# Performance work log

Measured on AMD Instinct MI355X. Metric: run time of the kernel, lower is better.

The kernel has to match this reference:

```python
import jax, jax.numpy as jnp
import numpy as np

B, H, W, D = 8, 32, 32, 384      # batch, height, width, channels (=dim)
E, HID, O = 8, 1536, 384         # num_experts, mlp hidden (dim*4), out_dim
TOP_K = 2


def setup_inputs() -> dict:
    key = jax.random.key(0)
    ks = jax.random.split(key, 5)
    x = jax.random.normal(ks[0], (B, H, W, D), dtype=jnp.float32)
    # router (noise_linear unused: eval path, train=False)
    Wg = 0.02 * jax.random.normal(ks[1], (D, E), dtype=jnp.float32)
    bg = jnp.zeros((E,), dtype=jnp.float32)
    # per-expert MLP params stacked along expert axis
    W1 = 0.02 * jax.random.normal(ks[2], (E, D, HID), dtype=jnp.float32)
    b1 = jnp.zeros((E, HID), dtype=jnp.float32)
    W2 = 0.02 * jax.random.normal(ks[3], (E, HID, O), dtype=jnp.float32)
    b2 = jnp.zeros((E, O), dtype=jnp.float32)
    return {"x": x, "Wg": Wg, "bg": bg, "W1": W1, "b1": b1, "W2": W2, "b2": b2}


def reference(x, Wg, bg, W1, b1, W2, b2):
    # --- NoisyTopkRouter (eval: train=False -> no noise branch) ---
    logits = jnp.einsum('bhwd,de->bhwe', x, Wg) + bg            # [B,H,W,E]
    _, top_idx = jax.lax.top_k(logits, TOP_K)                   # [B,H,W,K]
    # mask of selected experts; sparse logits = logits where selected, -inf else
    sel = jnp.sum(jax.nn.one_hot(top_idx, E, dtype=jnp.float32), axis=-2) > 0
    sparse_logits = jnp.where(sel, logits, -jnp.inf)
    gates = jax.nn.softmax(sparse_logits, axis=-1)              # zero on non-top-k

    # --- experts: since gate is exactly 0 off the top-k, the masked
    # gather-MLP-scatter loop equals a gate-weighted sum of all expert MLPs ---
    h = jnp.einsum('bhwd,edf->bhwef', x, W1) + b1               # [B,H,W,E,HID]
    h = jax.nn.gelu(h, approximate=False)                       # torch nn.GELU = exact
    y = jnp.einsum('bhwef,efo->bhweo', h, W2) + b2              # [B,H,W,E,O]
    out = jnp.einsum('bhweo,bhwe->bhwo', y, gates)              # [B,H,W,O]
    return out
```

## Files before the change

kernel.cpp:

```cpp
#include <hip/hip_runtime.h>
#include <cmath>

#define N_TOK 8192
#define DIM   384
#define NEXP  8
#define HID   1536
#define OUTD  384
#define CAP_MT 72
#define CAP_TOK 2304
#define CAP_TB 18

typedef __attribute__((ext_vector_type(8)))  __bf16 bf16x8;
typedef __attribute__((ext_vector_type(16))) float  f32x16;
typedef __attribute__((ext_vector_type(4)))  float  f32x4;
typedef __attribute__((ext_vector_type(8)))  unsigned short u16x8;

__device__ __forceinline__ unsigned short f2bf(float f) {
    unsigned u = __float_as_uint(f);
    u += 0x7FFF + ((u >> 16) & 1);
    return (unsigned short)(u >> 16);
}

__device__ __forceinline__ float bf2f(unsigned short s) {
    return __uint_as_float(((unsigned)s) << 16);
}

__device__ __forceinline__ float gelu_exact(float x) {
    return 0.5f * x * (1.0f + erff(x * 0.70710678118654752f));
}

__device__ __forceinline__ void cp16(const unsigned short* g, unsigned short* l) {
    __builtin_amdgcn_global_load_lds(
        (const __attribute__((address_space(1))) unsigned int*)g,
        (__attribute__((address_space(3))) unsigned int*)l, 16, 0, 0);
}

__global__ void swizzle_kernel(const float* __restrict__ W1, const float* __restrict__ W2,
                               unsigned short* __restrict__ w1s, unsigned short* __restrict__ w2s,
                               int* __restrict__ cnt) {
    if (blockIdx.x == 0 && threadIdx.x < NEXP) cnt[threadIdx.x] = 0;
    int gid = blockIdx.x * blockDim.x + threadIdx.x;
    const int T1 = NEXP * 48 * 24 * 64;
    const int T2 = NEXP * 12 * 96 * 64;
    const float* src; unsigned short* dst; int K, N, NT, KT, g;
    if (gid < T1)           { src = W1; dst = w1s; K = DIM; N = HID;  NT = 48; KT = 24; g = gid; }
    else if (gid < T1 + T2) { src = W2; dst = w2s; K = HID; N = OUTD; NT = 12; KT = 96; g = gid - T1; }
    else return;
    int l  = g & 63;
    int kt = (g >> 6) % KT;
    int nt = ((g >> 6) / KT) % NT;
    int e  = g / (64 * KT * NT);
    const float* s = src + ((size_t)e * K + kt * 16 + (l >> 5) * 8) * N + nt * 32 + (l & 31);
    unsigned short r[8];
    #pragma unroll
    for (int j = 0; j < 8; ++j) r[j] = f2bf(s[(size_t)j * N]);
    *(uint4*)(dst + (size_t)g * 8) = *(uint4*)r;
}

__global__ void router_kernel(const float* __restrict__ x, const float* __restrict__ Wg,
                              const float* __restrict__ bg, int* __restrict__ cnt,
                              int* __restrict__ btok, int* __restrict__ tokmap,
                              float* __restrict__ gmap, unsigned short* __restrict__ xb) {
    __shared__ float WgL[NEXP * DIM];
    __shared__ int lcnt[NEXP];
    __shared__ int lbase[NEXP];
    int tid = threadIdx.x;
    for (int i = tid; i < DIM * NEXP; i += 256) {
        int ch = i >> 3, e = i & 7;
        WgL[e * DIM + ch] = Wg[i];
    }
    if (tid < NEXP) lcnt[tid] = 0;
    __syncthreads();

    int tl  = tid >> 3;
    int seg = tid & 7;
    int t   = blockIdx.x * 32 + tl;

    float lg[NEXP] = {0.f, 0.f, 0.f, 0.f, 0.f, 0.f, 0.f, 0.f};
    const float* xr = x + (size_t)t * DIM;
    #pragma unroll
    for (int d4 = 0; d4 < 12; ++d4) {
        float4 v = *(const float4*)(xr + d4 * 32 + seg * 4);
        #pragma unroll
        for (int e = 0; e < NEXP; ++e) {
            float4 w = *(const float4*)&WgL[e * DIM + d4 * 32 + seg * 4];
            lg[e] += v.x * w.x + v.y * w.y + v.z * w.z + v.w * w.w;
        }
        unsigned short rr[4] = {f2bf(v.x), f2bf(v.y), f2bf(v.z), f2bf(v.w)};
        *(uint2*)(xb + (size_t)t * DIM + d4 * 32 + seg * 4) = *(uint2*)rr;
    }
    #pragma unroll
    for (int off = 1; off < 8; off <<= 1)
        #pragma unroll
        for (int e = 0; e < NEXP; ++e)
            lg[e] += __shfl_xor(lg[e], off);

    int p0 = 0, p1 = 0, i0 = 0, i1 = 0;
    float g0 = 0.f, g1 = 0.f;
    if (seg == 0) {
        float v0 = -INFINITY, v1 = -INFINITY;
        #pragma unroll
        for (int e = 0; e < NEXP; ++e) {
            float v = lg[e] + bg[e];
            if (v > v0)      { v1 = v0; i1 = i0; v0 = v; i0 = e; }
            else if (v > v1) { v1 = v;  i1 = e; }
        }
        float e1 = expf(v1 - v0);
        g0 = 1.f / (1.f + e1);
        g1 = e1  / (1.f + e1);
        p0 = atomicAdd(&lcnt[i0], 1);
        p1 = atomicAdd(&lcnt[i1], 1);
    }
    __syncthreads();
    if (tid < NEXP) lbase[tid] = atomicAdd(&cnt[tid], lcnt[tid]);
    __syncthreads();
    if (seg == 0) {
        int o0 = lbase[i0] + p0, o1 = lbase[i1] + p1;
        btok[i0 * N_TOK + o0] = t;
        btok[i1 * N_TOK + o1] = t;
        ((int4*)tokmap)[t] = make_int4(i0, o0, i1, o1);
        ((float2*)gmap)[t] = make_float2(g0, g1);
    }
}

__global__ void gather_kernel(const unsigned short* __restrict__ xb,
                              const int* __restrict__ cnt,
                              const int* __restrict__ btok, unsigned short* __restrict__ xg) {
    int mt = blockIdx.x, e = blockIdx.y;
    int cntE = cnt[e];
    if (mt * 32 >= cntE) return;
    int tid = threadIdx.x;
    int m = tid & 31, kt0 = tid >> 5;
    int pos = mt * 32 + m;
    int idx = (pos < cntE) ? pos : cntE - 1;
    int tok = btok[e * N_TOK + idx];
    const unsigned short* xr = xb + (size_t)tok * DIM;
    #pragma unroll
    for (int kk = 0; kk < 3; ++kk) {
        int kt = kt0 + kk * 8;
        #pragma unroll
        for (int kh = 0; kh < 2; ++kh) {
            uint4 v = *(const uint4*)(xr + kt * 16 + kh * 8);
            *(uint4*)(xg + (size_t)(((e * CAP_MT + mt) * 24 + kt) * 64 + kh * 32 + m) * 8) = v;
        }
    }
}

__global__ __launch_bounds__(512, 4) void gemm1_kernel(
        const unsigned short* __restrict__ xg, const unsigned short* __restrict__ w1s,
        const float* __restrict__ b1, const int* __restrict__ cnt,
        unsigned short* __restrict__ h) {
    int L = blockIdx.x;
    int e = L & 7;
    int r = L >> 3;
    int nb = r % 12;
    int tb = r / 12;
    int cntE = cnt[e];
    if (tb * 128 >= cntE) return;

    __shared__ unsigned short stg[3][12288];

    int tid = threadIdx.x;
    int wave = tid >> 6, lane = tid & 63;
    int m31 = lane & 31, kh = lane >> 5;
    int wm = wave & 1;
    int wn = wave >> 1;

    f32x16 acc[2];
    acc[0] = (f32x16){0.f,0.f,0.f,0.f,0.f,0.f,0.f,0.f,0.f,0.f,0.f,0.f,0.f,0.f,0.f,0.f};
    acc[1] = acc[0];

    const unsigned short* xa = xg  + ((size_t)(e * CAP_MT + tb * 4) * 24) * 512;
    const unsigned short* wb = w1s + ((size_t)(e * 48 + nb * 4) * 24) * 512;

    const unsigned short* sbase = (wave < 4)
        ? xa + ((size_t)wave * 24) * 512 + lane * 8
        : wb + ((size_t)(wave - 4) * 24) * 512 + lane * 8;
    int tbase = (wave < 4) ? wave * 3 : 12 + (wave - 4) * 3;

    auto issue = [&](int ks) {
        unsigned short* dst = &stg[ks % 3][tbase * 512];
        const unsigned short* sk = sbase + (size_t)ks * 1536;
        #pragma unroll
        for (int q = 0; q < 3; ++q)
            cp16(sk + q * 512, dst + q * 512);
    };
    auto consume = [&](int ks) {
        const unsigned short* bufp = stg[ks % 3];
        #pragma unroll
        for (int kt = 0; kt < 3; ++kt) {
            bf16x8 b  = *(const bf16x8*)&bufp[(12 + wn * 3 + kt) * 512 + lane * 8];
            bf16x8 a0 = *(const bf16x8*)&bufp[((wm * 2 + 0) * 3 + kt) * 512 + lane * 8];
            bf16x8 a1 = *(const bf16x8*)&bufp[((wm * 2 + 1) * 3 + kt) * 512 + lane * 8];
            acc[0] = __builtin_amdgcn_mfma_f32_32x32x16_bf16(a0, b, acc[0], 0, 0, 0);
            acc[1] = __builtin_amdgcn_mfma_f32_32x32x16_bf16(a1, b, acc[1], 0, 0, 0);
        }
    };

    issue(0); issue(1);
    for (int ks = 0; ks < 7; ++ks) {
        asm volatile("s_waitcnt vmcnt(3) lgkmcnt(0)" ::: "memory");
        __builtin_amdgcn_sched_barrier(0);
        __builtin_amdgcn_s_barrier();
        __builtin_amdgcn_sched_barrier(0);
        if (ks + 2 < 8) issue(ks + 2);
        consume(ks);
    }
    asm volatile("s_waitcnt vmcnt(0) lgkmcnt(0)" ::: "memory");
    __builtin_amdgcn_sched_barrier(0);
    __builtin_amdgcn_s_barrier();
    __builtin_amdgcn_sched_barrier(0);
    consume(7);

    __syncthreads();
    char* hw = (char*)stg + wave * 5120;
    float bv = b1[e * HID + nb * 128 + wn * 32 + m31];
    #pragma unroll
    for (int s = 0; s < 2; ++s)
        #pragma unroll
        for (int rr = 0; rr < 16; ++rr) {
            int rowl = s * 32 + (rr & 3) + 8 * (rr >> 2) + 4 * kh;
            *(unsigned short*)(hw + rowl * 80 + m31 * 2) = f2bf(gelu_exact(acc[s][rr] + bv));
        }
    #pragma unroll
    for (int mtl = 0; mtl < 2; ++mtl)
        #pragma unroll
        for (int ktl = 0; ktl < 2; ++ktl) {
            uint4 v = *(const uint4*)(hw + (mtl * 32 + m31) * 80 + (ktl * 16 + kh * 8) * 2);
            int mt = tb * 4 + wm * 2 + mtl;
            int kt = nb * 8 + wn * 2 + ktl;
            *(uint4*)(h + ((size_t)((e * CAP_MT + mt) * 96 + kt)) * 512 + lane * 8) = v;
        }
}

__global__ __launch_bounds__(512, 4) void gemm2_kernel(
        const unsigned short* __restrict__ h, const unsigned short* __restrict__ w2s,
        const int* __restrict__ cnt, unsigned short* __restrict__ yp) {
    int L = blockIdx.x;
    int e = L & 7;
    int r = L >> 3;
    int nb = r % 3;
    int tb = r / 3;
    int cntE = cnt[e];
    if (tb * 128 >= cntE) return;

    __shared__ unsigned short stg[3][12288];

    int tid = threadIdx.x;
    int wave = tid >> 6, lane = tid & 63;
    int m31 = lane & 31, kh = lane >> 5;
    int wm = wave & 1;
    int wn = wave >> 1;

    f32x16 acc[2];
    acc[0] = (f32x16){0.f,0.f,0.f,0.f,0.f,0.f,0.f,0.f,0.f,0.f,0.f,0.f,0.f,0.f,0.f,0.f};
    acc[1] = acc[0];

    const unsigned short* xa = h   + ((size_t)(e * CAP_MT + tb * 4) * 96) * 512;
    const unsigned short* wb = w2s + ((size_t)(e * 12 + nb * 4) * 96) * 512;

    const unsigned short* sbase = (wave < 4)
        ? xa + ((size_t)wave * 96) * 512 + lane * 8
        : wb + ((size_t)(wave - 4) * 96) * 512 + lane * 8;
    int tbase = (wave < 4) ? wave * 3 : 12 + (wave - 4) * 3;

    auto issue = [&](int ks) {
        unsigned short* dst = &stg[ks % 3][tbase * 512];
        const unsigned short* sk = sbase + (size_t)ks * 1536;
        #pragma unroll
        for (int q = 0; q < 3; ++q)
            cp16(sk + q * 512, dst + q * 512);
    };
    auto consume = [&](int ks) {
        const unsigned short* bufp = stg[ks % 3];
        #pragma unroll
        for (int kt = 0; kt < 3; ++kt) {
            bf16x8 b  = *(const bf16x8*)&bufp[(12 + wn * 3 + kt) * 512 + lane * 8];
            bf16x8 a0 = *(const bf16x8*)&bufp[((wm * 2 + 0) * 3 + kt) * 512 + lane * 8];
            bf16x8 a1 = *(const bf16x8*)&bufp[((wm * 2 + 1) * 3 + kt) * 512 + lane * 8];
            acc[0] = __builtin_amdgcn_mfma_f32_32x32x16_bf16(a0, b, acc[0], 0, 0, 0);
            acc[1] = __builtin_amdgcn_mfma_f32_32x32x16_bf16(a1, b, acc[1], 0, 0, 0);
        }
    };

    issue(0); issue(1);
    for (int ks = 0; ks < 31; ++ks) {
        asm volatile("s_waitcnt vmcnt(3) lgkmcnt(0)" ::: "memory");
        __builtin_amdgcn_sched_barrier(0);
        __builtin_amdgcn_s_barrier();
        __builtin_amdgcn_sched_barrier(0);
        if (ks + 2 < 32) issue(ks + 2);
        consume(ks);
    }
    asm volatile("s_waitcnt vmcnt(0) lgkmcnt(0)" ::: "memory");
    __builtin_amdgcn_sched_barrier(0);
    __builtin_amdgcn_s_barrier();
    __builtin_amdgcn_sched_barrier(0);
    consume(31);

    __syncthreads();
    char* hw = (char*)stg + wave * 4096;
    #pragma unroll
    for (int s = 0; s < 2; ++s)
        #pragma unroll
        for (int rr = 0; rr < 16; ++rr) {
            int rowl = s * 32 + (rr & 3) + 8 * (rr >> 2) + 4 * kh;
            *(unsigned short*)(hw + rowl * 64 + m31 * 2) = f2bf(acc[s][rr]);
        }
    #pragma unroll
    for (int it = 0; it < 4; ++it) {
        int rowl = it * 16 + (lane >> 2);
        int cc   = lane & 3;
        uint4 v = *(const uint4*)(hw + rowl * 64 + cc * 16);
        int pos = tb * 128 + wm * 64 + rowl;
        *(uint4*)(yp + (size_t)(e * CAP_TOK + pos) * OUTD + nb * 128 + wn * 32 + cc * 8) = v;
    }
}

__global__ void reduce_kernel(const unsigned short* __restrict__ yp,
                              const int* __restrict__ tokmap, const float* __restrict__ gmap,
                              const float* __restrict__ b2, float* __restrict__ out) {
    int gid = blockIdx.x * 256 + threadIdx.x;
    int t = gid / 48, q = gid - t * 48;
    int4   tm = ((const int4*)tokmap)[t];
    float2 g  = ((const float2*)gmap)[t];
    const unsigned short* p0 = yp + ((size_t)(tm.x * CAP_TOK + tm.y)) * OUTD + q * 8;
    const unsigned short* p1 = yp + ((size_t)(tm.z * CAP_TOK + tm.w)) * OUTD + q * 8;
    u16x8 a = __builtin_nontemporal_load((const u16x8*)p0);
    u16x8 b = __builtin_nontemporal_load((const u16x8*)p1);
    const float* c0 = &b2[tm.x * OUTD + q * 8];
    const float* c1 = &b2[tm.z * OUTD + q * 8];
    f32x4 r0, r1;
    #pragma unroll
    for (int j = 0; j < 4; ++j) {
        r0[j] = g.x * (bf2f(a[j]) + c0[j]) + g.y * (bf2f(b[j]) + c1[j]);
        r1[j] = g.x * (bf2f(a[4 + j]) + c0[4 + j]) + g.y * (bf2f(b[4 + j]) + c1[4 + j]);
    }
    float* op = &out[(size_t)t * OUTD + q * 8];
    __builtin_nontemporal_store(r0, (f32x4*)op);
    __builtin_nontemporal_store(r1, (f32x4*)(op + 4));
}

extern "C" void kernel_launch(void* const* d_in, const int* in_sizes, int n_in,
                              void* d_out, int out_size, void* d_ws, size_t ws_size,
                              hipStream_t stream) {
    const float* x  = (const float*)d_in[0];
    const float* Wg = (const float*)d_in[1];
    const float* bg = (const float*)d_in[2];
    const float* W1 = (const float*)d_in[3];
    const float* b1 = (const float*)d_in[4];
    const float* W2 = (const float*)d_in[5];
    const float* b2 = (const float*)d_in[6];
    float* out = (float*)d_out;

    char* ws = (char*)d_ws;
    int*            cnt    = (int*)ws;
    int*            btok   = (int*)(ws + 1024);
    int*            tokmap = (int*)(ws + 263168);
    float*          gmap   = (float*)(ws + 394240);
    unsigned short* xg     = (unsigned short*)(ws + 459776);
    unsigned short* w1s    = (unsigned short*)(ws + 14615552);
    unsigned short* w2s    = (unsigned short*)(ws + 24052736);
    unsigned short* h      = (unsigned short*)(ws + 33489920);
    unsigned short* xb     = (unsigned short*)(ws + 90113024);
    unsigned short* yp     = xg;

    hipLaunchKernelGGL(swizzle_kernel, dim3(4608), dim3(256), 0, stream,
                       W1, W2, w1s, w2s, cnt);
    hipLaunchKernelGGL(router_kernel, dim3(N_TOK / 32), dim3(256), 0, stream,
                       x, Wg, bg, cnt, btok, tokmap, gmap, xb);
    hipLaunchKernelGGL(gather_kernel, dim3(CAP_MT, NEXP), dim3(256), 0, stream,
                       xb, cnt, btok, xg);
    hipLaunchKernelGGL(gemm1_kernel, dim3(NEXP * 12 * CAP_TB), dim3(512), 0, stream,
                       xg, w1s, b1, cnt, h);
    hipLaunchKernelGGL(gemm2_kernel, dim3(NEXP * 3 * CAP_TB), dim3(512), 0, stream,
                       h, w2s, cnt, yp);
    hipLaunchKernelGGL(reduce_kernel, dim3(N_TOK * 48 / 256), dim3(256), 0, stream,
                       yp, tokmap, gmap, b2, out);
}
```

Before: 182.1 us.

## Retile expert GEMMs so each wave computes a 2x2 MFMA block

GEMM1 grows its token tile from 128 to 256 rows per block, and each of its 8 waves now computes a 64x64 sub-tile with a 2x2 grid of MFMA accumulators. This halves the GEMM1 grid and raises operand reuse from LDS. GEMM2 moves to 256-thread blocks of 4 waves, each wave also doing a 2x2 MFMA block over a 128x128 tile. GEMM2 uses a K-step of 32 with 48 pipeline stages and an adjusted vmcnt wait. The goal is to cut LDS reads per MFMA and staging overhead, at the cost of more accumulator registers per wave, possibly lower occupancy, and padded epilogue buffers read in 8-byte pieces.

```diff
diff --git a/kernel.cpp b/kernel.cpp
--- a/kernel.cpp
+++ b/kernel.cpp
@@ -8,7 +8,6 @@
 #define OUTD  384
 #define CAP_MT 72
 #define CAP_TOK 2304
-#define CAP_TB 18
 
 typedef __attribute__((ext_vector_type(8)))  __bf16 bf16x8;
 typedef __attribute__((ext_vector_type(16))) float  f32x16;
@@ -156,84 +155,99 @@
     int nb = r % 12;
     int tb = r / 12;
     int cntE = cnt[e];
-    if (tb * 128 >= cntE) return;
+    if (tb * 256 >= cntE) return;
 
     __shared__ unsigned short stg[3][12288];
 
     int tid = threadIdx.x;
     int wave = tid >> 6, lane = tid & 63;
     int m31 = lane & 31, kh = lane >> 5;
-    int wm = wave & 1;
-    int wn = wave >> 1;
-
-    f32x16 acc[2];
-    acc[0] = (f32x16){0.f,0.f,0.f,0.f,0.f,0.f,0.f,0.f,0.f,0.f,0.f,0.f,0.f,0.f,0.f,0.f};
-    acc[1] = acc[0];
-
-    const unsigned short* xa = xg  + ((size_t)(e * CAP_MT + tb * 4) * 24) * 512;
+    int wm = wave & 3;
+    int wn = wave >> 2;
+
+    f32x16 acc[2][2];
+    #pragma unroll
+    for (int i = 0; i < 2; ++i)
+        #pragma unroll
+        for (int j = 0; j < 2; ++j)
+            acc[i][j] = (f32x16){0.f,0.f,0.f,0.f,0.f,0.f,0.f,0.f,0.f,0.f,0.f,0.f,0.f,0.f,0.f,0.f};
+
+    const unsigned short* xa = xg  + ((size_t)(e * CAP_MT + tb * 8) * 24) * 512;
     const unsigned short* wb = w1s + ((size_t)(e * 48 + nb * 4) * 24) * 512;
 
-    const unsigned short* sbase = (wave < 4)
-        ? xa + ((size_t)wave * 24) * 512 + lane * 8
-        : wb + ((size_t)(wave - 4) * 24) * 512 + lane * 8;
-    int tbase = (wave < 4) ? wave * 3 : 12 + (wave - 4) * 3;
+    int wk = wave & 1, wh = wave >> 1;
+    const unsigned short* srcA1 = xa + ((size_t)wh * 24 + wk) * 512 + lane * 8;
+    const unsigned short* srcA2 = srcA1 + (size_t)4 * 24 * 512;
+    const unsigned short* srcB  = wb + ((size_t)wh * 24 + wk) * 512 + lane * 8;
 
     auto issue = [&](int ks) {
-        unsigned short* dst = &stg[ks % 3][tbase * 512];
-        const unsigned short* sk = sbase + (size_t)ks * 1536;
-        #pragma unroll
-        for (int q = 0; q < 3; ++q)
-            cp16(sk + q * 512, dst + q * 512);
+        unsigned short* buf = stg[ks % 3];
+        size_t off = (size_t)ks * 1024;
+        cp16(srcA1 + off, buf + wave * 512);
+        cp16(srcA2 + off, buf + (wave + 8) * 512);
+        cp16(srcB  + off, buf + (16 + wave) * 512);
     };
     auto consume = [&](int ks) {
-        const unsigned short* bufp = stg[ks % 3];
-        #pragma unroll
-        for (int kt = 0; kt < 3; ++kt) {
-            bf16x8 b  = *(const bf16x8*)&bufp[(12 + wn * 3 + kt) * 512 + lane * 8];
-            bf16x8 a0 = *(const bf16x8*)&bufp[((wm * 2 + 0) * 3 + kt) * 512 + lane * 8];
-            bf16x8 a1 = *(const bf16x8*)&bufp[((wm * 2 + 1) * 3 + kt) * 512 + lane * 8];
-            acc[0] = __builtin_amdgcn_mfma_f32_32x32x16_bf16(a0, b, acc[0], 0, 0, 0);
-            acc[1] = __builtin_amdgcn_mfma_f32_32x32x16_bf16(a1, b, acc[1], 0, 0, 0);
+        const unsigned short* buf = stg[ks % 3];
+        #pragma unroll
+        for (int kt = 0; kt < 2; ++kt) {
+            bf16x8 a0  = *(const bf16x8*)&buf[((wm * 2 + 0) * 2 + kt) * 512 + lane * 8];
+            bf16x8 a1  = *(const bf16x8*)&buf[((wm * 2 + 1) * 2 + kt) * 512 + lane * 8];
+            bf16x8 b0  = *(const bf16x8*)&buf[(16 + (wn * 2 + 0) * 2 + kt) * 512 + lane * 8];
+            bf16x8 b1v = *(const bf16x8*)&buf[(16 + (wn * 2 + 1) * 2 + kt) * 512 + lane * 8];
+            acc[0][0] = __builtin_amdgcn_mfma_f32_32x32x16_bf16(a0, b0,  acc[0][0], 0, 0, 0);
+            acc[0][1] = __builtin_amdgcn_mfma_f32_32x32x16_bf16(a0, b1v, acc[0][1], 0, 0, 0);
+            acc[1][0] = __builtin_amdgcn_mfma_f32_32x32x16_bf16(a1, b0,  acc[1][0], 0, 0, 0);
+            acc[1][1] = __builtin_amdgcn_mfma_f32_32x32x16_bf16(a1, b1v, acc[1][1], 0, 0, 0);
         }
     };
 
     issue(0); issue(1);
-    for (int ks = 0; ks < 7; ++ks) {
+    for (int ks = 0; ks < 11; ++ks) {
         asm volatile("s_waitcnt vmcnt(3) lgkmcnt(0)" ::: "memory");
         __builtin_amdgcn_sched_barrier(0);
         __builtin_amdgcn_s_barrier();
         __builtin_amdgcn_sched_barrier(0);
-        if (ks + 2 < 8) issue(ks + 2);
+        if (ks + 2 < 12) issue(ks + 2);
         consume(ks);
     }
     asm volatile("s_waitcnt vmcnt(0) lgkmcnt(0)" ::: "memory");
     __builtin_amdgcn_sched_barrier(0);
     __builtin_amdgcn_s_barrier();
     __builtin_amdgcn_sched_barrier(0);
-    consume(7);
+    consume(11);
 
     __syncthreads();
-    char* hw = (char*)stg + wave * 5120;
-    float bv = b1[e * HID + nb * 128 + wn * 32 + m31];
-    #pragma unroll
-    for (int s = 0; s < 2; ++s)
-        #pragma unroll
-        for (int rr = 0; rr < 16; ++rr) {
-            int rowl = s * 32 + (rr & 3) + 8 * (rr >> 2) + 4 * kh;
-            *(unsigned short*)(hw + rowl * 80 + m31 * 2) = f2bf(gelu_exact(acc[s][rr] + bv));
+    char* hw = (char*)stg + wave * 8704;
+    float bv0 = b1[e * HID + nb * 128 + wn * 64 + m31];
+    float bv1 = b1[e * HID + nb * 128 + wn * 64 + 32 + m31];
+    #pragma unroll
+    for (int im = 0; im < 2; ++im)
+        #pragma unroll
+        for (int in = 0; in < 2; ++in) {
+            float bv = in ? bv1 : bv0;
+            #pragma unroll
+            for (int rr = 0; rr < 16; ++rr) {
+                int rowl = im * 32 + (rr & 3) + 8 * (rr >> 2) + 4 * kh;
+                *(unsigned short*)(hw + rowl * 136 + (in * 32 + m31) * 2) =
+                    f2bf(gelu_exact(acc[im][in][rr] + bv));
+            }
         }
     #pragma unroll
     for (int mtl = 0; mtl < 2; ++mtl)
         #pragma unroll
-        for (int ktl = 0; ktl < 2; ++ktl) {
-            uint4 v = *(const uint4*)(hw + (mtl * 32 + m31) * 80 + (ktl * 16 + kh * 8) * 2);
-            int mt = tb * 4 + wm * 2 + mtl;
-            int kt = nb * 8 + wn * 2 + ktl;
+        for (int ktl = 0; ktl < 4; ++ktl) {
+            const char* p = hw + (mtl * 32 + m31) * 136 + (ktl * 16 + kh * 8) * 2;
+            uint2 v0 = *(const uint2*)p;
+            uint2 v1 = *(const uint2*)(p + 8);
+            uint4 v = make_uint4(v0.x, v0.y, v1.x, v1.y);
+            int mt = tb * 8 + wm * 2 + mtl;
+            int kt = nb * 8 + wn * 4 + ktl;
             *(uint4*)(h + ((size_t)((e * CAP_MT + mt) * 96 + kt)) * 512 + lane * 8) = v;
         }
 }
 
-__global__ __launch_bounds__(512, 4) void gemm2_kernel(
+__global__ __launch_bounds__(256, 3) void gemm2_kernel(
         const unsigned short* __restrict__ h, const unsigned short* __restrict__ w2s,
         const int* __restrict__ cnt, unsigned short* __restrict__ yp) {
     int L = blockIdx.x;
@@ -244,7 +258,7 @@
     int cntE = cnt[e];
     if (tb * 128 >= cntE) return;
 
-    __shared__ unsigned short stg[3][12288];
+    __shared__ unsigned short stg[3][8192];
 
     int tid = threadIdx.x;
     int wave = tid >> 6, lane = tid & 63;
@@ -252,68 +266,82 @@
     int wm = wave & 1;
     int wn = wave >> 1;
 
-    f32x16 acc[2];
-    acc[0] = (f32x16){0.f,0.f,0.f,0.f,0.f,0.f,0.f,0.f,0.f,0.f,0.f,0.f,0.f,0.f,0.f,0.f};
-    acc[1] = acc[0];
+    f32x16 acc[2][2];
+    #pragma unroll
+    for (int i = 0; i < 2; ++i)
+        #pragma unroll
+        for (int j = 0; j < 2; ++j)
+            acc[i][j] = (f32x16){0.f,0.f,0.f,0.f,0.f,0.f,0.f,0.f,0.f,0.f,0.f,0.f,0.f,0.f,0.f,0.f};
 
     const unsigned short* xa = h   + ((size_t)(e * CAP_MT + tb * 4) * 96) * 512;
     const unsigned short* wb = w2s + ((size_t)(e * 12 + nb * 4) * 96) * 512;
 
-    const unsigned short* sbase = (wave < 4)
-        ? xa + ((size_t)wave * 96) * 512 + lane * 8
-        : wb + ((size_t)(wave - 4) * 96) * 512 + lane * 8;
-    int tbase = (wave < 4) ? wave * 3 : 12 + (wave - 4) * 3;
+    int wk = wave & 1, wh = wave >> 1;
+    const unsigned short* srcA1 = xa + ((size_t)wh * 96 + wk) * 512 + lane * 8;
+    const unsigned short* srcA2 = srcA1 + (size_t)2 * 96 * 512;
+    const unsigned short* srcB1 = wb + ((size_t)wh * 96 + wk) * 512 + lane * 8;
+    const unsigned short* srcB2 = srcB1 + (size_t)2 * 96 * 512;
 
     auto issue = [&](int ks) {
-        unsigned short* dst = &stg[ks % 3][tbase * 512];
-        const unsigned short* sk = sbase + (size_t)ks * 1536;
-        #pragma unroll
-        for (int q = 0; q < 3; ++q)
-            cp16(sk + q * 512, dst + q * 512);
+        unsigned short* buf = stg[ks % 3];
+        size_t off = (size_t)ks * 1024;
+        cp16(srcA1 + off, buf + wave * 512);
+        cp16(srcA2 + off, buf + (wave + 4) * 512);
+        cp16(srcB1 + off, buf + (8 + wave) * 512);
+        cp16(srcB2 + off, buf + (8 + wave + 4) * 512);
     };
     auto consume = [&](int ks) {
-        const unsigned short* bufp = stg[ks % 3];
-        #pragma unroll
-        for (int kt = 0; kt < 3; ++kt) {
-            bf16x8 b  = *(const bf16x8*)&bufp[(12 + wn * 3 + kt) * 512 + lane * 8];
-            bf16x8 a0 = *(const bf16x8*)&bufp[((wm * 2 + 0) * 3 + kt) * 512 + lane * 8];
-            bf16x8 a1 = *(const bf16x8*)&bufp[((wm * 2 + 1) * 3 + kt) * 512 + lane * 8];
-            acc[0] = __builtin_amdgcn_mfma_f32_32x32x16_bf16(a0, b, acc[0], 0, 0, 0);
-            acc[1] = __builtin_amdgcn_mfma_f32_32x32x16_bf16(a1, b, acc[1], 0, 0, 0);
+        const unsigned short* buf = stg[ks % 3];
+        #pragma unroll
+        for (int kt = 0; kt < 2; ++kt) {
+            bf16x8 a0  = *(const bf16x8*)&buf[((wm * 2 + 0) * 2 + kt) * 512 + lane * 8];
+            bf16x8 a1  = *(const bf16x8*)&buf[((wm * 2 + 1) * 2 + kt) * 512 + lane * 8];
+            bf16x8 b0  = *(const bf16x8*)&buf[(8 + (wn * 2 + 0) * 2 + kt) * 512 + lane * 8];
+            bf16x8 b1v = *(const bf16x8*)&buf[(8 + (wn * 2 + 1) * 2 + kt) * 512 + lane * 8];
+            acc[0][0] = __builtin_amdgcn_mfma_f32_32x32x16_bf16(a0, b0,  acc[0][0], 0, 0, 0);
+            acc[0][1] = __builtin_amdgcn_mfma_f32_32x32x16_bf16(a0, b1v, acc[0][1], 0, 0, 0);
+            acc[1][0] = __builtin_amdgcn_mfma_f32_32x32x16_bf16(a1, b0,  acc[1][0], 0, 0, 0);
+            acc[1][1] = __builtin_amdgcn_mfma_f32_32x32x16_bf16(a1, b1v, acc[1][1], 0, 0, 0);
         }
     };
 
     issue(0); issue(1);
-    for (int ks = 0; ks < 31; ++ks) {
-        asm volatile("s_waitcnt vmcnt(3) lgkmcnt(0)" ::: "memory");
+    for (int ks = 0; ks < 47; ++ks) {
+        asm volatile("s_waitcnt vmcnt(4) lgkmcnt(0)" ::: "memory");
         __builtin_amdgcn_sched_barrier(0);
         __builtin_amdgcn_s_barrier();
         __builtin_amdgcn_sched_barrier(0);
-        if (ks + 2 < 32) issue(ks + 2);
+        if (ks + 2 < 48) issue(ks + 2);
         consume(ks);
     }
     asm volatile("s_waitcnt vmcnt(0) lgkmcnt(0)" ::: "memory");
     __builtin_amdgcn_sched_barrier(0);
     __builtin_amdgcn_s_barrier();
     __builtin_amdgcn_sched_barrier(0);
-    consume(31);
+    consume(47);
 
     __syncthreads();
-    char* hw = (char*)stg + wave * 4096;
-    #pragma unroll
-    for (int s = 0; s < 2; ++s)
-        #pragma unroll
-        for (int rr = 0; rr < 16; ++rr) {
-            int rowl = s * 32 + (rr & 3) + 8 * (rr >> 2) + 4 * kh;
-            *(unsigned short*)(hw + rowl * 64 + m31 * 2) = f2bf(acc[s][rr]);
-        }
-    #pragma unroll
-    for (int it = 0; it < 4; ++it) {
-        int rowl = it * 16 + (lane >> 2);
-        int cc   = lane & 3;
-        uint4 v = *(const uint4*)(hw + rowl * 64 + cc * 16);
+    char* hw = (char*)stg + wave * 8704;
+    #pragma unroll
+    for (int im = 0; im < 2; ++im)
+        #pragma unroll
+        for (int in = 0; in < 2; ++in)
+            #pragma unroll
+            for (int rr = 0; rr < 16; ++rr) {
+                int rowl = im * 32 + (rr & 3) + 8 * (rr >> 2) + 4 * kh;
+                *(unsigned short*)(hw + rowl * 136 + (in * 32 + m31) * 2) =
+                    f2bf(acc[im][in][rr]);
+            }
+    #pragma unroll
+    for (int it = 0; it < 8; ++it) {
+        int rowl = it * 8 + (lane >> 3);
+        int cc   = lane & 7;
+        const char* p = hw + rowl * 136 + cc * 16;
+        uint2 v0 = *(const uint2*)p;
+        uint2 v1 = *(const uint2*)(p + 8);
+        uint4 v = make_uint4(v0.x, v0.y, v1.x, v1.y);
         int pos = tb * 128 + wm * 64 + rowl;
-        *(uint4*)(yp + (size_t)(e * CAP_TOK + pos) * OUTD + nb * 128 + wn * 32 + cc * 8) = v;
+        *(uint4*)(yp + (size_t)(e * CAP_TOK + pos) * OUTD + nb * 128 + wn * 64 + cc * 8) = v;
     }
 }
 
@@ -371,9 +399,9 @@
                        x, Wg, bg, cnt, btok, tokmap, gmap, xb);
     hipLaunchKernelGGL(gather_kernel, dim3(CAP_MT, NEXP), dim3(256), 0, stream,
                        xb, cnt, btok, xg);
-    hipLaunchKernelGGL(gemm1_kernel, dim3(NEXP * 12 * CAP_TB), dim3(512), 0, stream,
+    hipLaunchKernelGGL(gemm1_kernel, dim3(NEXP * 12 * 9), dim3(512), 0, stream,
                        xg, w1s, b1, cnt, h);
-    hipLaunchKernelGGL(gemm2_kernel, dim3(NEXP * 3 * CAP_TB), dim3(512), 0, stream,
+    hipLaunchKernelGGL(gemm2_kernel, dim3(NEXP * 3 * 18), dim3(256), 0, stream,
                        h, w2s, cnt, yp);
     hipLaunchKernelGGL(reduce_kernel, dim3(N_TOK * 48 / 256), dim3(256), 0, stream,
                        yp, tokmap, gmap, b2, out);
```

Result: no change. 181.5 us (-0.3%).
